# Performance work log

Hardware: AMD Instinct MI355X
Metric: run time of the kernel (lower is better)

## Reference

```python
import jax, jax.numpy as jnp
import numpy as np

N_NODES = 100000
N_EDGES = 1600000
N_FEAT = 128
N_CLASSES = 10
N_GRAPHS = 256


def setup_inputs() -> dict:
    key = jax.random.key(0)
    ks = jax.random.split(key, 16)
    x = jax.random.normal(ks[0], (N_NODES, N_FEAT), dtype=jnp.float32)
    edge_index = jax.random.randint(ks[1], (2, N_EDGES), 0, N_NODES, dtype=jnp.int64)
    batch = jnp.sort(jax.random.randint(ks[2], (N_NODES,), 0, N_GRAPHS, dtype=jnp.int64))
    s = 0.1
    # GAT1: in=128 -> heads=8, out_per_head=8, concat -> 64
    W1 = jax.random.normal(ks[3], (N_FEAT, 64), dtype=jnp.float32) * s
    a_src1 = jax.random.normal(ks[4], (8, 8), dtype=jnp.float32) * s
    a_dst1 = jax.random.normal(ks[5], (8, 8), dtype=jnp.float32) * s
    b1 = jnp.zeros((64,), jnp.float32)
    # GAT2: in=64 -> heads=1, out=128
    W2 = jax.random.normal(ks[6], (64, 128), dtype=jnp.float32) * s
    a_src2 = jax.random.normal(ks[7], (1, 128), dtype=jnp.float32) * s
    a_dst2 = jax.random.normal(ks[8], (1, 128), dtype=jnp.float32) * s
    b2 = jnp.zeros((128,), jnp.float32)
    fc_w = jax.random.normal(ks[9], (128, N_CLASSES), dtype=jnp.float32) * s
    fc_b = jnp.zeros((N_CLASSES,), jnp.float32)
    return {"x": x, "edge_index": edge_index, "batch": batch,
            "W1": W1, "a_src1": a_src1, "a_dst1": a_dst1, "b1": b1,
            "W2": W2, "a_src2": a_src2, "a_dst2": a_dst2, "b2": b2,
            "fc_w": fc_w, "fc_b": fc_b}


def _segment_softmax(e, seg, n):
    # e: [E, H]; softmax over edges sharing the same destination node
    m = jax.ops.segment_max(e, seg, num_segments=n)
    m = jnp.where(jnp.isfinite(m), m, jnp.zeros_like(m))  # guard isolated nodes
    ex = jnp.exp(e - m[seg])
    s = jax.ops.segment_sum(ex, seg, num_segments=n)
    return ex / (s[seg] + jnp.asarray(1e-16, e.dtype))


def _gat_conv(x, src, dst, W, a_src, a_dst, bias):
    # PyG GATConv (eval mode, self-loops already appended to src/dst)
    H, C = a_src.shape
    n = x.shape[0]
    h = (x @ W).reshape(n, H, C)                      # [N,H,C]
    al_s = jnp.einsum('nhc,hc->nh', h, a_src)          # [N,H]
    al_d = jnp.einsum('nhc,hc->nh', h, a_dst)
    e = jax.nn.leaky_relu(al_s[src] + al_d[dst], 0.2)  # [E,H]
    alpha = _segment_softmax(e, dst, n)                # [E,H]
    out = jax.ops.segment_sum(h[src] * alpha[..., None], dst, num_segments=n)  # [N,H,C]
    return out.reshape(n, H * C) + bias                # concat=True (H=1 layer2 is identity reshape)


def reference(x, edge_index, batch, W1, a_src1, a_dst1, b1, W2, a_src2, a_dst2, b2, fc_w, fc_b):
    n = x.shape[0]
    loop = jnp.arange(n, dtype=edge_index.dtype)
    src = jnp.concatenate([edge_index[0], loop])       # add self-loops (PyG default)
    dst = jnp.concatenate([edge_index[1], loop])
    x1 = jax.nn.relu(_gat_conv(x, src, dst, W1, a_src1, a_dst1, b1))
    # dropout p=0.6 is identity in eval mode
    x2 = _gat_conv(x1, src, dst, W2, a_src2, a_dst2, b2)
    cnt = jax.ops.segment_sum(jnp.ones((n,), x2.dtype), batch, num_segments=N_GRAPHS)
    pooled = jax.ops.segment_sum(x2, batch, num_segments=N_GRAPHS) / jnp.maximum(cnt, 1.0)[:, None]
    logits = pooled @ fc_w + fc_b
    return jax.nn.log_softmax(logits, axis=1)
```

## Files before the change

kernel.cpp:

```cpp
#include <hip/hip_runtime.h>
#include <math.h>

typedef unsigned int uint;
typedef unsigned short ushort;
typedef unsigned char uchar;
typedef __attribute__((ext_vector_type(2))) float v2f;

#define S1 4.0f
#define S2 16.0f

template <bool HI>
__device__ inline v2f fp8x2f(uint u) {
    return __builtin_amdgcn_cvt_pk_f32_fp8((int)u, HI);
}

__global__ __launch_bounds__(256) void k_gemm1(const float* __restrict__ x,
                                               const float* __restrict__ W1,
                                               const float* __restrict__ as1,
                                               const float* __restrict__ ad1,
                                               uchar* __restrict__ h1f8,
                                               float* __restrict__ al1s,
                                               float* __restrict__ al1d, int N) {
    __shared__ float sB[128 * 64];
    __shared__ float sA[64 * 68];
    const int t = threadIdx.x;
    const int n0 = blockIdx.x * 64;
    {
        const float4* w4 = (const float4*)W1;
        float4* s4 = (float4*)sB;
#pragma unroll
        for (int i = 0; i < 8; ++i) s4[t + i * 256] = w4[t + i * 256];
    }
    const int r0 = (t >> 3) * 2;
    const int c0 = (t & 7) * 8;
    float acc0[8] = {0, 0, 0, 0, 0, 0, 0, 0};
    float acc1[8] = {0, 0, 0, 0, 0, 0, 0, 0};
    for (int kb = 0; kb < 2; ++kb) {
        __syncthreads();
#pragma unroll
        for (int i = 0; i < 4; ++i) {
            int idx = t + i * 256;
            int r = idx >> 4, kc = idx & 15;
            int n = n0 + r;
            float4 v = make_float4(0.f, 0.f, 0.f, 0.f);
            if (n < N) v = ((const float4*)x)[(size_t)n * 32 + kb * 16 + kc];
            *(float4*)&sA[r * 68 + kc * 4] = v;
        }
        __syncthreads();
        const float* bptr = &sB[kb * 64 * 64];
#pragma unroll 8
        for (int kk = 0; kk < 64; ++kk) {
            float a0 = sA[r0 * 68 + kk];
            float a1 = sA[(r0 + 1) * 68 + kk];
            const float* bp = &bptr[kk * 64 + c0];
            float4 b0 = *(const float4*)bp;
            float4 b1v = *(const float4*)(bp + 4);
            acc0[0] += a0 * b0.x; acc0[1] += a0 * b0.y; acc0[2] += a0 * b0.z; acc0[3] += a0 * b0.w;
            acc0[4] += a0 * b1v.x; acc0[5] += a0 * b1v.y; acc0[6] += a0 * b1v.z; acc0[7] += a0 * b1v.w;
            acc1[0] += a1 * b0.x; acc1[1] += a1 * b0.y; acc1[2] += a1 * b0.z; acc1[3] += a1 * b0.w;
            acc1[4] += a1 * b1v.x; acc1[5] += a1 * b1v.y; acc1[6] += a1 * b1v.z; acc1[7] += a1 * b1v.w;
        }
    }
    float ps0 = 0.f, pd0 = 0.f, ps1 = 0.f, pd1 = 0.f;
#pragma unroll
    for (int i = 0; i < 8; ++i) {
        float ws = as1[c0 + i], wd = ad1[c0 + i];
        ps0 += acc0[i] * ws; pd0 += acc0[i] * wd;
        ps1 += acc1[i] * ws; pd1 += acc1[i] * wd;
    }
    int n = n0 + r0;
    int head = t & 7;
    if (n < N) {
        int q0 = 0, q1 = 0;
        q0 = __builtin_amdgcn_cvt_pk_fp8_f32(acc0[0] * S1, acc0[1] * S1, q0, false);
        q0 = __builtin_amdgcn_cvt_pk_fp8_f32(acc0[2] * S1, acc0[3] * S1, q0, true);
        q1 = __builtin_amdgcn_cvt_pk_fp8_f32(acc0[4] * S1, acc0[5] * S1, q1, false);
        q1 = __builtin_amdgcn_cvt_pk_fp8_f32(acc0[6] * S1, acc0[7] * S1, q1, true);
        uint2 p; p.x = (uint)q0; p.y = (uint)q1;
        *(uint2*)&h1f8[(size_t)n * 64 + c0] = p;
        al1s[(size_t)n * 8 + head] = ps0;
        al1d[(size_t)n * 8 + head] = pd0;
    }
    if (n + 1 < N) {
        int q0 = 0, q1 = 0;
        q0 = __builtin_amdgcn_cvt_pk_fp8_f32(acc1[0] * S1, acc1[1] * S1, q0, false);
        q0 = __builtin_amdgcn_cvt_pk_fp8_f32(acc1[2] * S1, acc1[3] * S1, q0, true);
        q1 = __builtin_amdgcn_cvt_pk_fp8_f32(acc1[4] * S1, acc1[5] * S1, q1, false);
        q1 = __builtin_amdgcn_cvt_pk_fp8_f32(acc1[6] * S1, acc1[7] * S1, q1, true);
        uint2 p; p.x = (uint)q0; p.y = (uint)q1;
        *(uint2*)&h1f8[(size_t)(n + 1) * 64 + c0] = p;
        al1s[(size_t)(n + 1) * 8 + head] = ps1;
        al1d[(size_t)(n + 1) * 8 + head] = pd1;
    }
}

__global__ __launch_bounds__(256) void k_gemm2(const float* __restrict__ x1pre,
                                               const float* __restrict__ W2,
                                               const float* __restrict__ b1,
                                               const float* __restrict__ as2,
                                               const float* __restrict__ ad2,
                                               uchar* __restrict__ h2f8,
                                               float* __restrict__ al2s,
                                               float* __restrict__ al2d, int N) {
    __shared__ float sB[64 * 128];
    __shared__ float sA[64 * 68];
    const int t = threadIdx.x;
    const int n0 = blockIdx.x * 64;
    {
        const float4* w4 = (const float4*)W2;
        float4* s4 = (float4*)sB;
#pragma unroll
        for (int i = 0; i < 8; ++i) s4[t + i * 256] = w4[t + i * 256];
    }
#pragma unroll
    for (int i = 0; i < 4; ++i) {
        int idx = t + i * 256;
        int r = idx >> 4, kc = idx & 15;
        int n = n0 + r;
        float4 v = make_float4(0.f, 0.f, 0.f, 0.f);
        if (n < N) {
            v = ((const float4*)x1pre)[(size_t)n * 16 + kc];
            float4 bb = ((const float4*)b1)[kc];
            v.x = fmaxf(v.x + bb.x, 0.f);
            v.y = fmaxf(v.y + bb.y, 0.f);
            v.z = fmaxf(v.z + bb.z, 0.f);
            v.w = fmaxf(v.w + bb.w, 0.f);
        }
        *(float4*)&sA[r * 68 + kc * 4] = v;
    }
    __syncthreads();
    const int r0 = (t >> 3) * 2;
    const int cb = (t & 7) * 4;
    float acc0[16], acc1[16];
#pragma unroll
    for (int i = 0; i < 16; ++i) { acc0[i] = 0.f; acc1[i] = 0.f; }
#pragma unroll 4
    for (int k = 0; k < 64; ++k) {
        float a0 = sA[r0 * 68 + k];
        float a1 = sA[(r0 + 1) * 68 + k];
#pragma unroll
        for (int j = 0; j < 4; ++j) {
            float4 b = *(const float4*)&sB[k * 128 + cb + 32 * j];
            acc0[j * 4 + 0] += a0 * b.x; acc0[j * 4 + 1] += a0 * b.y;
            acc0[j * 4 + 2] += a0 * b.z; acc0[j * 4 + 3] += a0 * b.w;
            acc1[j * 4 + 0] += a1 * b.x; acc1[j * 4 + 1] += a1 * b.y;
            acc1[j * 4 + 2] += a1 * b.z; acc1[j * 4 + 3] += a1 * b.w;
        }
    }
    float ps0 = 0.f, pd0 = 0.f, ps1 = 0.f, pd1 = 0.f;
#pragma unroll
    for (int j = 0; j < 4; ++j)
#pragma unroll
        for (int i = 0; i < 4; ++i) {
            int cc = cb + 32 * j + i;
            float ws = as2[cc], wd = ad2[cc];
            ps0 += acc0[j * 4 + i] * ws; pd0 += acc0[j * 4 + i] * wd;
            ps1 += acc1[j * 4 + i] * ws; pd1 += acc1[j * 4 + i] * wd;
        }
#pragma unroll
    for (int off = 1; off < 8; off <<= 1) {
        ps0 += __shfl_xor(ps0, off); pd0 += __shfl_xor(pd0, off);
        ps1 += __shfl_xor(ps1, off); pd1 += __shfl_xor(pd1, off);
    }
    int n = n0 + r0;
    if (n < N) {
#pragma unroll
        for (int j = 0; j < 4; ++j) {
            int q = 0;
            q = __builtin_amdgcn_cvt_pk_fp8_f32(acc0[j * 4 + 0] * S2, acc0[j * 4 + 1] * S2, q, false);
            q = __builtin_amdgcn_cvt_pk_fp8_f32(acc0[j * 4 + 2] * S2, acc0[j * 4 + 3] * S2, q, true);
            *(uint*)&h2f8[(size_t)n * 128 + cb + 32 * j] = (uint)q;
        }
        if ((t & 7) == 0) { al2s[n] = ps0; al2d[n] = pd0; }
    }
    if (n + 1 < N) {
#pragma unroll
        for (int j = 0; j < 4; ++j) {
            int q = 0;
            q = __builtin_amdgcn_cvt_pk_fp8_f32(acc1[j * 4 + 0] * S2, acc1[j * 4 + 1] * S2, q, false);
            q = __builtin_amdgcn_cvt_pk_fp8_f32(acc1[j * 4 + 2] * S2, acc1[j * 4 + 3] * S2, q, true);
            *(uint*)&h2f8[(size_t)(n + 1) * 128 + cb + 32 * j] = (uint)q;
        }
        if ((t & 7) == 0) { al2s[n + 1] = ps1; al2d[n + 1] = pd1; }
    }
}

__global__ __launch_bounds__(256) void k_deg(const int* __restrict__ dst,
                                             int* __restrict__ deg,
                                             int* __restrict__ rank, int E) {
    int base = (blockIdx.x * 256 + threadIdx.x) * 4;
    if (base + 4 <= E) {
        int4 d = *(const int4*)&dst[base];
        int r0 = atomicAdd(&deg[d.x], 1);
        int r1 = atomicAdd(&deg[d.y], 1);
        int r2 = atomicAdd(&deg[d.z], 1);
        int r3 = atomicAdd(&deg[d.w], 1);
        *(int4*)&rank[base] = make_int4(r0, r1, r2, r3);
    } else {
        for (int e = base; e < E; ++e) {
            int d = dst[e];
            rank[e] = atomicAdd(&deg[d], 1);
        }
    }
}

__global__ void k_scan1(const int* __restrict__ deg, int* __restrict__ row_ptr,
                        int* __restrict__ bsums, int N) {
    __shared__ int sh[256];
    int t = threadIdx.x, b = blockIdx.x;
    int i = b * 256 + t;
    int v = (i < N) ? (deg[i] + 1) : 0;
    sh[t] = v;
    __syncthreads();
    int accv = v;
    for (int off = 1; off < 256; off <<= 1) {
        int u = (t >= off) ? sh[t - off] : 0;
        __syncthreads();
        accv += u;
        sh[t] = accv;
        __syncthreads();
    }
    if (i < N) row_ptr[i] = accv - v;
    if (t == 255) bsums[b] = accv;
}

__global__ void k_scan2(int* __restrict__ bsums, int nb) {
    __shared__ int sh[512];
    int t = threadIdx.x;
    int v = (t < nb) ? bsums[t] : 0;
    sh[t] = v;
    __syncthreads();
    int accv = v;
    for (int off = 1; off < 512; off <<= 1) {
        int u = (t >= off) ? sh[t - off] : 0;
        __syncthreads();
        accv += u;
        sh[t] = accv;
        __syncthreads();
    }
    if (t < nb) bsums[t] = accv - v;
}

__global__ void k_scan3(int* __restrict__ row_ptr, const int* __restrict__ bsums,
                        const int* __restrict__ deg, int* __restrict__ col,
                        int N, int total) {
    int i = blockIdx.x * 256 + threadIdx.x;
    if (i < N) {
        int rp = row_ptr[i] + bsums[blockIdx.x];
        row_ptr[i] = rp;
        col[rp + deg[i]] = i;
    }
    if (i == 0) row_ptr[N] = total;
}

__global__ __launch_bounds__(256) void k_fill(const int* __restrict__ src,
                                              const int* __restrict__ dst,
                                              const int* __restrict__ rank,
                                              const int* __restrict__ row_ptr,
                                              int* __restrict__ col, int E) {
    int base = (blockIdx.x * 256 + threadIdx.x) * 4;
    if (base + 4 <= E) {
        int4 d = *(const int4*)&dst[base];
        int4 s = *(const int4*)&src[base];
        int4 r = *(const int4*)&rank[base];
        int p0 = row_ptr[d.x] + r.x;
        int p1 = row_ptr[d.y] + r.y;
        int p2 = row_ptr[d.z] + r.z;
        int p3 = row_ptr[d.w] + r.w;
        col[p0] = s.x;
        col[p1] = s.y;
        col[p2] = s.z;
        col[p3] = s.w;
    } else {
        for (int e = base; e < E; ++e) col[row_ptr[dst[e]] + rank[e]] = src[e];
    }
}

__global__ __launch_bounds__(256) void k_edge1(const uchar* __restrict__ h1f8,
                                               const float* __restrict__ al1s,
                                               const float* __restrict__ al1d,
                                               const int* __restrict__ row_ptr,
                                               const int* __restrict__ col,
                                               float* __restrict__ x1pre, int N) {
    int node = blockIdx.x * 4 + (threadIdx.x >> 6);
    if (node >= N) return;
    const int lane = threadIdx.x & 63;
    const int e8 = lane >> 3;
    const int h = lane & 7;
    const int g = lane >> 4;
    const int k4 = lane & 15;
    const int hh = k4 >> 1;
    float a_d = al1d[(size_t)node * 8 + h];
    const int s0 = row_ptr[node], s1 = row_ptr[node + 1];
    float den_part = 0.f;
    float acc[4] = {0.f, 0.f, 0.f, 0.f};
    for (int base = s0; base < s1; base += 64) {
        int idx = base + lane;
        int cidx = idx < s1 ? idx : s1 - 1;
        int my_col = col[cidx];
        int cnt = s1 - base; if (cnt > 64) cnt = 64;
        int cntR = (cnt + 7) & ~7;
        int i = 0;
        for (; i + 16 <= cntR; i += 16) {
            int cA = __shfl(my_col, i + g);
            int cB = __shfl(my_col, i + 4 + g);
            int cC = __shfl(my_col, i + 8 + g);
            int cD = __shfl(my_col, i + 12 + g);
            uint hA = *(const uint*)(h1f8 + (size_t)cA * 64 + k4 * 4);
            uint hB = *(const uint*)(h1f8 + (size_t)cB * 64 + k4 * 4);
            uint hC = *(const uint*)(h1f8 + (size_t)cC * 64 + k4 * 4);
            uint hD = *(const uint*)(h1f8 + (size_t)cD * 64 + k4 * 4);
            int c0 = __shfl(my_col, i + e8);
            int c1 = __shfl(my_col, i + 8 + e8);
            float e0v = al1s[(size_t)c0 * 8 + h] + a_d;
            float e1v = al1s[(size_t)c1 * 8 + h] + a_d;
            e0v = e0v > 0.f ? e0v : 0.2f * e0v;
            e1v = e1v > 0.f ? e1v : 0.2f * e1v;
            float w0 = (base + i + e8 < s1) ? __expf(e0v) : 0.f;
            float w1 = (base + i + 8 + e8 < s1) ? __expf(e1v) : 0.f;
            den_part += w0 + w1;
            float wA = __shfl(w0, g * 8 + hh);
            float wB = __shfl(w0, (4 + g) * 8 + hh);
            float wC = __shfl(w1, g * 8 + hh);
            float wD = __shfl(w1, (4 + g) * 8 + hh);
            v2f p;
            p = fp8x2f<false>(hA); acc[0] += wA * p.x; acc[1] += wA * p.y;
            p = fp8x2f<true>(hA);  acc[2] += wA * p.x; acc[3] += wA * p.y;
            p = fp8x2f<false>(hB); acc[0] += wB * p.x; acc[1] += wB * p.y;
            p = fp8x2f<true>(hB);  acc[2] += wB * p.x; acc[3] += wB * p.y;
            p = fp8x2f<false>(hC); acc[0] += wC * p.x; acc[1] += wC * p.y;
            p = fp8x2f<true>(hC);  acc[2] += wC * p.x; acc[3] += wC * p.y;
            p = fp8x2f<false>(hD); acc[0] += wD * p.x; acc[1] += wD * p.y;
            p = fp8x2f<true>(hD);  acc[2] += wD * p.x; acc[3] += wD * p.y;
        }
        if (i < cntR) {
            int cA = __shfl(my_col, i + g);
            int cB = __shfl(my_col, i + 4 + g);
            uint hA = *(const uint*)(h1f8 + (size_t)cA * 64 + k4 * 4);
            uint hB = *(const uint*)(h1f8 + (size_t)cB * 64 + k4 * 4);
            int c0 = __shfl(my_col, i + e8);
            float e0v = al1s[(size_t)c0 * 8 + h] + a_d;
            e0v = e0v > 0.f ? e0v : 0.2f * e0v;
            float w0 = (base + i + e8 < s1) ? __expf(e0v) : 0.f;
            den_part += w0;
            float wA = __shfl(w0, g * 8 + hh);
            float wB = __shfl(w0, (4 + g) * 8 + hh);
            v2f p;
            p = fp8x2f<false>(hA); acc[0] += wA * p.x; acc[1] += wA * p.y;
            p = fp8x2f<true>(hA);  acc[2] += wA * p.x; acc[3] += wA * p.y;
            p = fp8x2f<false>(hB); acc[0] += wB * p.x; acc[1] += wB * p.y;
            p = fp8x2f<true>(hB);  acc[2] += wB * p.x; acc[3] += wB * p.y;
        }
    }
#pragma unroll
    for (int i = 0; i < 4; ++i) {
        acc[i] += __shfl_xor(acc[i], 16);
        acc[i] += __shfl_xor(acc[i], 32);
    }
    den_part += __shfl_xor(den_part, 8);
    den_part += __shfl_xor(den_part, 16);
    den_part += __shfl_xor(den_part, 32);
    float den = __shfl(den_part, hh);
    if (lane < 16) {
        float invd = 1.f / (den * S1);
        ((float4*)x1pre)[(size_t)node * 16 + k4] =
            make_float4(acc[0] * invd, acc[1] * invd, acc[2] * invd, acc[3] * invd);
    }
}

__global__ __launch_bounds__(256) void k_edge2(const uchar* __restrict__ h2f8,
                                               const float* __restrict__ al2s,
                                               const float* __restrict__ al2d,
                                               const int* __restrict__ row_ptr,
                                               const int* __restrict__ col,
                                               const float* __restrict__ b2,
                                               float* __restrict__ x2, int N) {
    int node = blockIdx.x * 4 + (threadIdx.x >> 6);
    if (node >= N) return;
    const int lane = threadIdx.x & 63;
    const int g = lane >> 4;
    const int k8 = lane & 15;
    float a_d = al2d[node];
    int s0 = row_ptr[node], s1 = row_ptr[node + 1];
    float acc[8];
#pragma unroll
    for (int i = 0; i < 8; ++i) acc[i] = 0.f;
    float den = 0.f;
    for (int base = s0; base < s1; base += 64) {
        int idx = base + lane;
        int cidx = idx < s1 ? idx : s1 - 1;
        int my_col = col[cidx];
        float my_e = al2s[my_col] + a_d;
        my_e = my_e > 0.f ? my_e : 0.2f * my_e;
        float my_w = (idx < s1) ? __expf(my_e) : 0.f;
        den += my_w;
        int cnt = s1 - base; if (cnt > 64) cnt = 64;
        int cntR = (cnt + 7) & ~7;
        int i = 0;
        for (; i + 16 <= cntR; i += 16) {
            int eA = i + g, eB = i + 4 + g, eC = i + 8 + g, eD = i + 12 + g;
            int cA = __shfl(my_col, eA), cB = __shfl(my_col, eB);
            int cC = __shfl(my_col, eC), cD = __shfl(my_col, eD);
            float wA = __shfl(my_w, eA), wB = __shfl(my_w, eB);
            float wC = __shfl(my_w, eC), wD = __shfl(my_w, eD);
            uint2 hA = *(const uint2*)(h2f8 + (size_t)cA * 128 + k8 * 8);
            uint2 hB = *(const uint2*)(h2f8 + (size_t)cB * 128 + k8 * 8);
            uint2 hC = *(const uint2*)(h2f8 + (size_t)cC * 128 + k8 * 8);
            uint2 hD = *(const uint2*)(h2f8 + (size_t)cD * 128 + k8 * 8);
            v2f p;
            p = fp8x2f<false>(hA.x); acc[0] += wA * p.x; acc[1] += wA * p.y;
            p = fp8x2f<true>(hA.x);  acc[2] += wA * p.x; acc[3] += wA * p.y;
            p = fp8x2f<false>(hA.y); acc[4] += wA * p.x; acc[5] += wA * p.y;
            p = fp8x2f<true>(hA.y);  acc[6] += wA * p.x; acc[7] += wA * p.y;
            p = fp8x2f<false>(hB.x); acc[0] += wB * p.x; acc[1] += wB * p.y;
            p = fp8x2f<true>(hB.x);  acc[2] += wB * p.x; acc[3] += wB * p.y;
            p = fp8x2f<false>(hB.y); acc[4] += wB * p.x; acc[5] += wB * p.y;
            p = fp8x2f<true>(hB.y);  acc[6] += wB * p.x; acc[7] += wB * p.y;
            p = fp8x2f<false>(hC.x); acc[0] += wC * p.x; acc[1] += wC * p.y;
            p = fp8x2f<true>(hC.x);  acc[2] += wC * p.x; acc[3] += wC * p.y;
            p = fp8x2f<false>(hC.y); acc[4] += wC * p.x; acc[5] += wC * p.y;
            p = fp8x2f<true>(hC.y);  acc[6] += wC * p.x; acc[7] += wC * p.y;
            p = fp8x2f<false>(hD.x); acc[0] += wD * p.x; acc[1] += wD * p.y;
            p = fp8x2f<true>(hD.x);  acc[2] += wD * p.x; acc[3] += wD * p.y;
            p = fp8x2f<false>(hD.y); acc[4] += wD * p.x; acc[5] += wD * p.y;
            p = fp8x2f<true>(hD.y);  acc[6] += wD * p.x; acc[7] += wD * p.y;
        }
        if (i < cntR) {
            int eA = i + g, eB = i + 4 + g;
            int cA = __shfl(my_col, eA), cB = __shfl(my_col, eB);
            float wA = __shfl(my_w, eA), wB = __shfl(my_w, eB);
            uint2 hA = *(const uint2*)(h2f8 + (size_t)cA * 128 + k8 * 8);
            uint2 hB = *(const uint2*)(h2f8 + (size_t)cB * 128 + k8 * 8);
            v2f p;
            p = fp8x2f<false>(hA.x); acc[0] += wA * p.x; acc[1] += wA * p.y;
            p = fp8x2f<true>(hA.x);  acc[2] += wA * p.x; acc[3] += wA * p.y;
            p = fp8x2f<false>(hA.y); acc[4] += wA * p.x; acc[5] += wA * p.y;
            p = fp8x2f<true>(hA.y);  acc[6] += wA * p.x; acc[7] += wA * p.y;
            p = fp8x2f<false>(hB.x); acc[0] += wB * p.x; acc[1] += wB * p.y;
            p = fp8x2f<true>(hB.x);  acc[2] += wB * p.x; acc[3] += wB * p.y;
            p = fp8x2f<false>(hB.y); acc[4] += wB * p.x; acc[5] += wB * p.y;
            p = fp8x2f<true>(hB.y);  acc[6] += wB * p.x; acc[7] += wB * p.y;
        }
    }
#pragma unroll
    for (int off = 1; off < 64; off <<= 1) den += __shfl_xor(den, off);
#pragma unroll
    for (int i = 0; i < 8; ++i) {
        acc[i] += __shfl_xor(acc[i], 16);
        acc[i] += __shfl_xor(acc[i], 32);
    }
    if (lane < 16) {
        float invd = 1.f / (den * S2);
        const float4* bb = (const float4*)b2;
        float4 o0 = bb[k8 * 2], o1 = bb[k8 * 2 + 1];
        float4* dst = (float4*)(x2 + (size_t)node * 128 + k8 * 8);
        dst[0] = make_float4(acc[0] * invd + o0.x, acc[1] * invd + o0.y,
                             acc[2] * invd + o0.z, acc[3] * invd + o0.w);
        dst[1] = make_float4(acc[4] * invd + o1.x, acc[5] * invd + o1.y,
                             acc[6] * invd + o1.z, acc[7] * invd + o1.w);
    }
}

__global__ __launch_bounds__(128) void k_pool(const float* __restrict__ x2,
                                              const int* __restrict__ batch,
                                              float* __restrict__ pooled,
                                              float* __restrict__ cnt, int N) {
    int t = threadIdx.x;
    int nstart = blockIdx.x * 128;
    if (nstart >= N) return;
    int nend = nstart + 128;
    if (nend > N) nend = N;
    float acc = 0.f;
    int cur = batch[nstart];
    int count = 0;
    for (int n = nstart; n < nend; ++n) {
        int g = batch[n];
        if (g != cur) {
            atomicAdd(&pooled[(size_t)cur * 128 + t], acc);
            if (t == 0) atomicAdd(&cnt[cur], (float)count);
            acc = 0.f;
            count = 0;
            cur = g;
        }
        acc += x2[(size_t)n * 128 + t];
        ++count;
    }
    atomicAdd(&pooled[(size_t)cur * 128 + t], acc);
    if (t == 0) atomicAdd(&cnt[cur], (float)count);
}

__global__ __launch_bounds__(64) void k_fc(const float* __restrict__ pooled,
                                           const float* __restrict__ cnt,
                                           const float* __restrict__ fcw,
                                           const float* __restrict__ fcb,
                                           float* __restrict__ out, int G) {
    int g = blockIdx.x;
    int c = threadIdx.x;
    float2 p = ((const float2*)pooled)[(size_t)g * 64 + c];
    float inv = 1.f / fmaxf(cnt[g], 1.f);
    p.x *= inv; p.y *= inv;
    float l[10];
#pragma unroll
    for (int j = 0; j < 10; ++j)
        l[j] = p.x * fcw[(2 * c) * 10 + j] + p.y * fcw[(2 * c + 1) * 10 + j];
#pragma unroll
    for (int j = 0; j < 10; ++j)
        for (int off = 1; off < 64; off <<= 1) l[j] += __shfl_xor(l[j], off);
    if (c == 0) {
        float lj[10];
        float m = -1e30f;
#pragma unroll
        for (int j = 0; j < 10; ++j) {
            lj[j] = l[j] + fcb[j];
            m = fmaxf(m, lj[j]);
        }
        float s = 0.f;
#pragma unroll
        for (int j = 0; j < 10; ++j) s += expf(lj[j] - m);
        float ls = logf(s);
#pragma unroll
        for (int j = 0; j < 10; ++j) out[(size_t)g * 10 + j] = lj[j] - m - ls;
    }
}

extern "C" void kernel_launch(void* const* d_in, const int* in_sizes, int n_in,
                              void* d_out, int out_size, void* d_ws, size_t ws_size,
                              hipStream_t stream) {
    const float* x     = (const float*)d_in[0];
    const int*   ei    = (const int*)d_in[1];
    const int*   batch = (const int*)d_in[2];
    const float* W1    = (const float*)d_in[3];
    const float* as1   = (const float*)d_in[4];
    const float* ad1   = (const float*)d_in[5];
    const float* b1    = (const float*)d_in[6];
    const float* W2    = (const float*)d_in[7];
    const float* as2   = (const float*)d_in[8];
    const float* ad2   = (const float*)d_in[9];
    const float* b2    = (const float*)d_in[10];
    const float* fcw   = (const float*)d_in[11];
    const float* fcb   = (const float*)d_in[12];
    float* out = (float*)d_out;

    const int N = in_sizes[0] / 128;
    const int E = in_sizes[1] / 2;
    const int G = out_size / 10;
    const int* srcp = ei;
    const int* dstp = ei + E;

    float* wf = (float*)d_ws;
    uchar* h1f8   = (uchar*)wf;
    float* x1pre  = wf + (size_t)N * 16;
    float* x2     = wf;
    uchar* h2f8   = (uchar*)(wf + (size_t)N * 128);
    float* al1s_  = wf + (size_t)N * 160;
    float* al1d_  = wf + (size_t)N * 168;
    float* al2s_  = wf + (size_t)N * 176;
    float* al2d_  = wf + (size_t)N * 177;
    float* pooled = wf + (size_t)N * 178;
    float* cnt    = pooled + (size_t)G * 128;
    int* deg      = (int*)(cnt + G);
    int* row_ptr  = deg + N;
    int* col      = row_ptr + N + 1;
    int* rank     = col + (size_t)E + N;
    int* bsums    = rank + E;

    size_t zbytes = ((size_t)G * 128 + G + (size_t)N) * sizeof(float);
    (void)hipMemsetAsync(pooled, 0, zbytes, stream);

    const int nb64 = (N + 63) / 64;
    const int nb4  = (N + 3) / 4;
    const int nbS  = (N + 255) / 256;
    const int nbP  = (N + 127) / 128;
    const int nbE4 = (E + 1023) / 1024;

    k_deg<<<nbE4, 256, 0, stream>>>(dstp, deg, rank, E);
    k_gemm1<<<nb64, 256, 0, stream>>>(x, W1, as1, ad1, h1f8, al1s_, al1d_, N);
    k_scan1<<<nbS, 256, 0, stream>>>(deg, row_ptr, bsums, N);
    k_scan2<<<1, 512, 0, stream>>>(bsums, nbS);
    k_scan3<<<nbS, 256, 0, stream>>>(row_ptr, bsums, deg, col, N, E + N);
    k_fill<<<nbE4, 256, 0, stream>>>(srcp, dstp, rank, row_ptr, col, E);
    k_edge1<<<nb4, 256, 0, stream>>>(h1f8, al1s_, al1d_, row_ptr, col, x1pre, N);
    k_gemm2<<<nb64, 256, 0, stream>>>(x1pre, W2, b1, as2, ad2, h2f8, al2s_, al2d_, N);
    k_edge2<<<nb4, 256, 0, stream>>>(h2f8, al2s_, al2d_, row_ptr, col, b2, x2, N);
    k_pool<<<nbP, 128, 0, stream>>>(x2, batch, pooled, cnt, N);
    k_fc<<<G, 64, 0, stream>>>(pooled, cnt, fcw, fcb, out, G);
}
```

Measured before the change: 400.8 us.

## Build CSR via two-level bucketed counting sort with shared-memory atomics

Replaces the global-atomic degree count, three-pass scan and scattered fill with a bucketed counting sort. Edges are first histogrammed into 128-node buckets per chunk using LDS atomics, then scanned and scattered into a bucket-ordered edge buffer. Each bucket is then turned into CSR rows with local atomics. This is meant to remove contended global atomics and the random global writes of the rank/fill passes, at the cost of an extra edge buffer pass and more kernel launches. Node-level ordering within a row becomes nondeterministic.

```diff
diff --git a/kernel.cpp b/kernel.cpp
--- a/kernel.cpp
+++ b/kernel.cpp
@@ -185,31 +185,112 @@
     }
 }
 
-__global__ __launch_bounds__(256) void k_deg(const int* __restrict__ dst,
-                                             int* __restrict__ deg,
-                                             int* __restrict__ rank, int E) {
-    int base = (blockIdx.x * 256 + threadIdx.x) * 4;
-    if (base + 4 <= E) {
-        int4 d = *(const int4*)&dst[base];
-        int r0 = atomicAdd(&deg[d.x], 1);
-        int r1 = atomicAdd(&deg[d.y], 1);
-        int r2 = atomicAdd(&deg[d.z], 1);
-        int r3 = atomicAdd(&deg[d.w], 1);
-        *(int4*)&rank[base] = make_int4(r0, r1, r2, r3);
-    } else {
-        for (int e = base; e < E; ++e) {
-            int d = dst[e];
-            rank[e] = atomicAdd(&deg[d], 1);
-        }
-    }
-}
-
-__global__ void k_scan1(const int* __restrict__ deg, int* __restrict__ row_ptr,
-                        int* __restrict__ bsums, int N) {
+
+__global__ __launch_bounds__(256) void k_hist(const int* __restrict__ dst,
+                                              int* __restrict__ counts,
+                                              int E, int CH, int NB) {
+    __shared__ int hist[784];
+    int t = threadIdx.x, b = blockIdx.x;
+    for (int k = t; k < NB; k += 256) hist[k] = 0;
+    __syncthreads();
+    int e0 = b * CH;
+    int e1 = e0 + CH; if (e1 > E) e1 = E;
+    for (int e = e0 + t; e < e1; e += 256)
+        atomicAdd(&hist[dst[e] >> 7], 1);
+    __syncthreads();
+    for (int k = t; k < NB; k += 256) counts[(size_t)b * NB + k] = hist[k];
+}
+
+__global__ __launch_bounds__(256) void k_bscan(int* __restrict__ counts,
+                                               int* __restrict__ btot,
+                                               int C, int NB) {
     __shared__ int sh[256];
+    int t = threadIdx.x, k = blockIdx.x;
+    int v[4];
+#pragma unroll
+    for (int i = 0; i < 4; ++i) {
+        int b = t * 4 + i;
+        v[i] = (b < C) ? counts[(size_t)b * NB + k] : 0;
+    }
+    int s = v[0] + v[1] + v[2] + v[3];
+    sh[t] = s;
+    __syncthreads();
+    int accv = s;
+    for (int off = 1; off < 256; off <<= 1) {
+        int u = (t >= off) ? sh[t - off] : 0;
+        __syncthreads();
+        accv += u;
+        sh[t] = accv;
+        __syncthreads();
+    }
+    int excl = accv - s;
+#pragma unroll
+    for (int i = 0; i < 4; ++i) {
+        int b = t * 4 + i;
+        if (b < C) counts[(size_t)b * NB + k] = excl;
+        excl += v[i];
+    }
+    if (t == 255) btot[k] = accv;
+}
+
+__global__ void k_bscan2(const int* __restrict__ btot, int* __restrict__ bbase,
+                         int NB, int E) {
+    __shared__ int sh[1024];
+    int t = threadIdx.x;
+    int v = (t < NB) ? btot[t] : 0;
+    sh[t] = v;
+    __syncthreads();
+    int accv = v;
+    for (int off = 1; off < 1024; off <<= 1) {
+        int u = (t >= off) ? sh[t - off] : 0;
+        __syncthreads();
+        accv += u;
+        sh[t] = accv;
+        __syncthreads();
+    }
+    if (t < NB) bbase[t] = accv - v;
+    if (t == 0) bbase[NB] = E;
+}
+
+__global__ __launch_bounds__(256) void k_bucket(const int* __restrict__ src,
+                                                const int* __restrict__ dst,
+                                                const int* __restrict__ counts,
+                                                const int* __restrict__ bbase,
+                                                int2* __restrict__ ebuf,
+                                                int E, int CH, int NB) {
+    __shared__ int pos[784];
     int t = threadIdx.x, b = blockIdx.x;
-    int i = b * 256 + t;
-    int v = (i < N) ? (deg[i] + 1) : 0;
+    for (int k = t; k < NB; k += 256)
+        pos[k] = bbase[k] + counts[(size_t)b * NB + k];
+    __syncthreads();
+    int e0 = b * CH;
+    int e1 = e0 + CH; if (e1 > E) e1 = E;
+    for (int e = e0 + t; e < e1; e += 256) {
+        int d = dst[e], s = src[e];
+        int p = atomicAdd(&pos[d >> 7], 1);
+        ebuf[p] = make_int2(s, d);
+    }
+}
+
+__global__ __launch_bounds__(256) void k_csr(const int* __restrict__ bbase,
+                                             const int2* __restrict__ ebuf,
+                                             int* __restrict__ row_ptr,
+                                             int* __restrict__ col,
+                                             int N, int E) {
+    __shared__ int cnt[128];
+    __shared__ int fill[128];
+    __shared__ int rowb[128];
+    __shared__ int sh[256];
+    int t = threadIdx.x, k = blockIdx.x;
+    int lo = bbase[k], hi = bbase[k + 1];
+    int nlo = k << 7;
+    int nn = N - nlo; if (nn > 128) nn = 128;
+    if (t < 128) { cnt[t] = 0; fill[t] = 0; }
+    __syncthreads();
+    for (int i = lo + t; i < hi; i += 256)
+        atomicAdd(&cnt[ebuf[i].y & 127], 1);
+    __syncthreads();
+    int v = (t < nn) ? (cnt[t] + 1) : 0;
     sh[t] = v;
     __syncthreads();
     int accv = v;
@@ -220,59 +301,20 @@
         sh[t] = accv;
         __syncthreads();
     }
-    if (i < N) row_ptr[i] = accv - v;
-    if (t == 255) bsums[b] = accv;
-}
-
-__global__ void k_scan2(int* __restrict__ bsums, int nb) {
-    __shared__ int sh[512];
-    int t = threadIdx.x;
-    int v = (t < nb) ? bsums[t] : 0;
-    sh[t] = v;
-    __syncthreads();
-    int accv = v;
-    for (int off = 1; off < 512; off <<= 1) {
-        int u = (t >= off) ? sh[t - off] : 0;
-        __syncthreads();
-        accv += u;
-        sh[t] = accv;
-        __syncthreads();
-    }
-    if (t < nb) bsums[t] = accv - v;
-}
-
-__global__ void k_scan3(int* __restrict__ row_ptr, const int* __restrict__ bsums,
-                        const int* __restrict__ deg, int* __restrict__ col,
-                        int N, int total) {
-    int i = blockIdx.x * 256 + threadIdx.x;
-    if (i < N) {
-        int rp = row_ptr[i] + bsums[blockIdx.x];
-        row_ptr[i] = rp;
-        col[rp + deg[i]] = i;
-    }
-    if (i == 0) row_ptr[N] = total;
-}
-
-__global__ __launch_bounds__(256) void k_fill(const int* __restrict__ src,
-                                              const int* __restrict__ dst,
-                                              const int* __restrict__ rank,
-                                              const int* __restrict__ row_ptr,
-                                              int* __restrict__ col, int E) {
-    int base = (blockIdx.x * 256 + threadIdx.x) * 4;
-    if (base + 4 <= E) {
-        int4 d = *(const int4*)&dst[base];
-        int4 s = *(const int4*)&src[base];
-        int4 r = *(const int4*)&rank[base];
-        int p0 = row_ptr[d.x] + r.x;
-        int p1 = row_ptr[d.y] + r.y;
-        int p2 = row_ptr[d.z] + r.z;
-        int p3 = row_ptr[d.w] + r.w;
-        col[p0] = s.x;
-        col[p1] = s.y;
-        col[p2] = s.z;
-        col[p3] = s.w;
-    } else {
-        for (int e = base; e < E; ++e) col[row_ptr[dst[e]] + rank[e]] = src[e];
+    int fbase = lo + nlo;
+    if (t < nn) {
+        int rb = fbase + accv - v;
+        rowb[t] = rb;
+        row_ptr[nlo + t] = rb;
+        col[rb + cnt[t]] = nlo + t;
+    }
+    if (k == 0 && t == 0) row_ptr[N] = E + N;
+    __syncthreads();
+    for (int i = lo + t; i < hi; i += 256) {
+        int2 e = ebuf[i];
+        int j = e.y & 127;
+        int r = atomicAdd(&fill[j], 1);
+        col[rowb[j] + r] = e.x;
     }
 }
 
@@ -558,27 +600,32 @@
     float* al2d_  = wf + (size_t)N * 177;
     float* pooled = wf + (size_t)N * 178;
     float* cnt    = pooled + (size_t)G * 128;
-    int* deg      = (int*)(cnt + G);
-    int* row_ptr  = deg + N;
-    int* col      = row_ptr + N + 1;
-    int* rank     = col + (size_t)E + N;
-    int* bsums    = rank + E;
-
-    size_t zbytes = ((size_t)G * 128 + G + (size_t)N) * sizeof(float);
+
+    const int NB = (N + 127) >> 7;
+    const int C  = 1024;
+    const int CH = (E + C - 1) / C;
+
+    int* ib = (int*)(((uintptr_t)(cnt + G) + 15) & ~(uintptr_t)15);
+    int2* ebuf   = (int2*)ib;
+    int* counts  = ib + 2 * (size_t)E;
+    int* btot    = counts + (size_t)C * NB;
+    int* bbase   = btot + NB;
+    int* row_ptr = bbase + NB + 1;
+    int* col     = row_ptr + N + 1;
+
+    size_t zbytes = ((size_t)G * 128 + G) * sizeof(float);
     (void)hipMemsetAsync(pooled, 0, zbytes, stream);
 
     const int nb64 = (N + 63) / 64;
     const int nb4  = (N + 3) / 4;
-    const int nbS  = (N + 255) / 256;
     const int nbP  = (N + 127) / 128;
-    const int nbE4 = (E + 1023) / 1024;
-
-    k_deg<<<nbE4, 256, 0, stream>>>(dstp, deg, rank, E);
+
+    k_hist<<<C, 256, 0, stream>>>(dstp, counts, E, CH, NB);
     k_gemm1<<<nb64, 256, 0, stream>>>(x, W1, as1, ad1, h1f8, al1s_, al1d_, N);
-    k_scan1<<<nbS, 256, 0, stream>>>(deg, row_ptr, bsums, N);
-    k_scan2<<<1, 512, 0, stream>>>(bsums, nbS);
-    k_scan3<<<nbS, 256, 0, stream>>>(row_ptr, bsums, deg, col, N, E + N);
-    k_fill<<<nbE4, 256, 0, stream>>>(srcp, dstp, rank, row_ptr, col, E);
+    k_bscan<<<NB, 256, 0, stream>>>(counts, btot, C, NB);
+    k_bscan2<<<1, 1024, 0, stream>>>(btot, bbase, NB, E);
+    k_bucket<<<C, 256, 0, stream>>>(srcp, dstp, counts, bbase, ebuf, E, CH, NB);
+    k_csr<<<NB, 256, 0, stream>>>(bbase, ebuf, row_ptr, col, N, E);
     k_edge1<<<nb4, 256, 0, stream>>>(h1f8, al1s_, al1d_, row_ptr, col, x1pre, N);
     k_gemm2<<<nb64, 256, 0, stream>>>(x1pre, W2, b1, as2, ad2, h2f8, al2s_, al2d_, N);
     k_edge2<<<nb4, 256, 0, stream>>>(h2f8, al2s_, al2d_, row_ptr, col, b2, x2, N);
```

Measured after the change: 362.9 us. -9.5%, faster.
